# Optimization experiments

Hardware: AMD Instinct MI355X
Metric: run time of the kernel (lower is better)

Reference implementation:

```python
import jax, jax.numpy as jnp
import numpy as np
from jax import lax

B, C, H, W = 16, 512, 16, 300
K, G = 8, 2          # k_clusters, g_clusters (gvlad)
OUT = 5994           # n speakers
DN = ('NCHW', 'OIHW', 'NCHW')


def setup_inputs() -> dict:
    key = jax.random.key(0)
    ks = jax.random.split(key, 10)
    s = lambda fan: 1.0 / np.sqrt(fan)
    return {
        'x5': jax.random.normal(ks[0], (B, C, H, W), jnp.float32),
        'x4': jnp.zeros((1, 1, 1, 1), jnp.float32),
        'x3': jnp.zeros((1, 1, 1, 1), jnp.float32),
        'x2': jnp.zeros((1, 1, 1, 1), jnp.float32),
        'x1': jnp.zeros((1, 1, 1, 1), jnp.float32),
        'conv_w': jax.random.normal(ks[1], (C, C, 7, 1), jnp.float32) * s(C * 7),
        'conv_b': jnp.zeros((C,), jnp.float32),
        'cc_w': jax.random.normal(ks[2], (K + G, C, 7, 1), jnp.float32) * s(C * 7),
        'cc_b': jnp.zeros((K + G,), jnp.float32),
        'centroids': jax.random.normal(ks[3], (K + G, C), jnp.float32),
        'fc_w': jax.random.normal(ks[4], (C, C * K), jnp.float32) * s(C * K),
        'fc_b': jnp.zeros((C,), jnp.float32),
        'logit_w': jax.random.normal(ks[5], (OUT, C), jnp.float32) * s(C),
    }


def _conv(x, w, b=None):
    y = lax.conv_general_dilated(x, w, (1, 1), 'VALID', dimension_numbers=DN)
    if b is not None:
        y = y + b[None, :, None, None]
    return y


def _forward(x5, conv_w, conv_b, cc_w, cc_b, centroids, fc_w, fc_b, logit_w):
    feats = jnp.maximum(_conv(x5, conv_w, conv_b), 0.0)      # (B,C,H',W) relu conv
    scores = _conv(x5, cc_w, cc_b)                           # (B,K+G,H',W)
    assign = jax.nn.softmax(scores, axis=1)                  # soft cluster assignment
    # VLAD: sum_hw a[b,k,h,w]*(f[b,c,h,w] - cent[k,c]), computed without
    # materializing the (B,K+G,C,H',W) residual tensor (same math, fused form)
    agg = jnp.einsum('bkhw,bchw->bkc', assign, feats)        # (B,K+G,C)
    asum = jnp.sum(assign, axis=(2, 3))                      # (B,K+G)
    cluster_res = agg - asum[:, :, None] * centroids[None]   # (B,K+G,C)
    cluster_res = cluster_res[:, :K, :]                      # gvlad: drop ghost clusters
    norm = jnp.linalg.norm(cluster_res, axis=-1, keepdims=True)
    cluster_l2 = cluster_res / jnp.maximum(norm, 1e-12)
    vlad = cluster_l2.reshape(-1, K * C)                     # (B, K*C)
    emb = jnp.maximum(vlad @ fc_w.T + fc_b, 0.0)             # (B,C)
    logit = emb @ logit_w.T                                  # (B,OUT)
    return emb, logit


def reference(x5, x4, x3, x2, x1, conv_w, conv_b, cc_w, cc_b, centroids,
              fc_w, fc_b, logit_w):
    # x4..x1 are unused by Decoder.forward (only x5 flows through)
    return _forward(x5, conv_w, conv_b, cc_w, cc_b, centroids, fc_w, fc_b, logit_w)
```

## Files before the change

### kernel.cpp

```cpp
#include <hip/hip_runtime.h>
#include <hip/hip_bf16.h>

typedef __attribute__((ext_vector_type(8))) short bf16x8;
typedef __attribute__((ext_vector_type(4))) float f32x4;

__device__ __forceinline__ void async16(const void* g, void* l) {
    __builtin_amdgcn_global_load_lds(
        (const __attribute__((address_space(1))) unsigned int*)g,
        (__attribute__((address_space(3))) unsigned int*)l, 16, 0, 0);
}

__global__ __launch_bounds__(256) void pack_all(const float* __restrict__ x5,
                                                const float* __restrict__ conv_w,
                                                const float* __restrict__ cc_w,
                                                __hip_bfloat16* __restrict__ X3,
                                                __hip_bfloat16* __restrict__ A2f) {
    __shared__ __align__(16) float smem[64 * 65];
    const int f = blockIdx.x;
    if (f < 10240) {
        float(*tile)[65] = (float(*)[65])smem;
        const int ct = f / 1280, r = f % 1280;
        const int wt = r >> 8, bh = r & 255;
        const int b = bh >> 4, h = bh & 15;
        const int w0 = wt * 64, c0 = ct * 64;
        const int lw = (threadIdx.x & 15) * 4;
        const int lc = threadIdx.x >> 4;
#pragma unroll
        for (int i = 0; i < 4; ++i) {
            const int c = lc + i * 16;
            const int w = w0 + lw;
            const float* src = &x5[((size_t)(b * 512 + c0 + c) * 16 + h) * 300 + w];
            float4 v = {0.f, 0.f, 0.f, 0.f};
            if (w + 3 < 300) v = *(const float4*)src;
            else {
                if (w < 300)     v.x = src[0];
                if (w + 1 < 300) v.y = src[1];
                if (w + 2 < 300) v.z = src[2];
            }
            *(float4*)&tile[c][lw] = v;
        }
        __syncthreads();
        const int sc = (threadIdx.x & 15) * 4;
        const int sw0 = threadIdx.x >> 4;
#pragma unroll
        for (int i = 0; i < 4; ++i) {
            const int wl = sw0 + i * 16;
            const int w = w0 + wl;
            if (w < 300) {
                __hip_bfloat16 p[4];
                p[0] = __float2bfloat16(tile[sc + 0][wl]);
                p[1] = __float2bfloat16(tile[sc + 1][wl]);
                p[2] = __float2bfloat16(tile[sc + 2][wl]);
                p[3] = __float2bfloat16(tile[sc + 3][wl]);
                *(uint2*)&X3[(((size_t)(b * 16 + h) * 300 + w)) * 512 + c0 + sc] = *(uint2*)p;
            }
        }
    } else {
        float* w = smem;
        const int co = f - 10240;
        if (co < 522) {
            const float4* src = (co < 512) ? (const float4*)(conv_w + (size_t)co * 3584)
                                           : (const float4*)(cc_w + (size_t)(co - 512) * 3584);
            for (int i = threadIdx.x; i < 896; i += 256) *(float4*)&w[i * 4] = src[i];
        } else {
            for (int i = threadIdx.x; i < 3584; i += 256) w[i] = 0.f;
        }
        __syncthreads();
        const int g = co >> 4, fl = co & 15;
        for (int chunk = threadIdx.x; chunk < 448; chunk += 256) {
            const int kk0 = chunk * 8;
            const int kt = kk0 >> 5, sq = (kk0 >> 3) & 3;
            __hip_bfloat16 p[8];
#pragma unroll
            for (int j = 0; j < 8; ++j) {
                const int k = kk0 + j;
                p[j] = __float2bfloat16(w[(k & 511) * 7 + (k >> 9)]);
            }
            char* dst = (char*)A2f + (((size_t)g * 112 + kt) * 64 + sq * 16 + fl) * 16;
            *(uint4*)dst = *(uint4*)p;
        }
    }
}

__global__ __launch_bounds__(256, 4) void conv_gemm(
    const __hip_bfloat16* __restrict__ A2f, const __hip_bfloat16* __restrict__ X3,
    const float* __restrict__ conv_b, const float* __restrict__ cc_b,
    __hip_bfloat16* __restrict__ feats, float* __restrict__ scores) {
    __shared__ __align__(16) char lds[16384];
    const int tid = threadIdx.x;
    const int wv = tid >> 6;
    const int lane = tid & 63;

    const int gid = blockIdx.x;
    const int xcd = gid & 7;
    const int j = gid >> 3;
    const int nb = xcd * 48 + j / 5;
    const int m0 = (j % 5) * 128;
    const int b = nb / 24;
    const int nt = nb % 24;

    const int row0 = wv * 16 + (lane >> 2);
    const int kseg = (lane & 3) ^ ((lane >> 3) & 3);
    int n0 = nt * 128 + row0;      if (n0 > 2999) n0 = 2999;
    int n1 = nt * 128 + row0 + 64; if (n1 > 2999) n1 = 2999;
    const char* gB0 = (const char*)X3 + ((size_t)((b * 16 + n0 / 300) * 300 + n0 % 300)) * 1024 + (size_t)kseg * 16;
    const char* gB1 = (const char*)X3 + ((size_t)((b * 16 + n1 / 300) * 300 + n1 % 300)) * 1024 + (size_t)kseg * 16;
    char* lB = lds + wv * 1024 + lane * 16;

    const int wm = (wv & 1) * 64;
    const int wn = (wv >> 1) * 64;
    const int fl = lane & 15;
    const int sq = lane >> 4;
    int boff[4];
#pragma unroll
    for (int i = 0; i < 4; ++i) {
        const int swz = (sq ^ ((fl >> 1) & 3)) * 16;
        boff[i] = (wn + i * 16 + fl) * 64 + swz;
    }
    const char* Af = (const char*)A2f;
    const int gb = (m0 >> 4) + ((wv & 1) << 2);

    f32x4 acc[4][4] = {};
    bf16x8 aC[4], aN[4];

#define ISSUE_B(kt, ph)                                                                \
    {                                                                                  \
        const size_t badd = (size_t)((kt) >> 4) * 307200 + (size_t)((kt) & 15) * 64;   \
        async16(gB0 + badd, lB + (ph) * 8192);                                         \
        async16(gB1 + badd, lB + (ph) * 8192 + 4096);                                  \
    }
#define PRE_A(kt, arr)                                                                 \
    {                                                                                  \
        _Pragma("unroll")                                                              \
        for (int mi = 0; mi < 4; ++mi)                                                 \
            arr[mi] = *(const bf16x8*)(Af + (((size_t)(gb + mi) * 112 + (kt)) << 10) + (lane << 4)); \
    }
#define COMPUTE(ph, arr)                                                               \
    {                                                                                  \
        _Pragma("unroll")                                                              \
        for (int ni = 0; ni < 4; ++ni) {                                               \
            const bf16x8 bv = *(const bf16x8*)(lds + (ph) * 8192 + boff[ni]);          \
            _Pragma("unroll")                                                          \
            for (int mi = 0; mi < 4; ++mi)                                             \
                acc[mi][ni] = __builtin_amdgcn_mfma_f32_16x16x32_bf16(arr[mi], bv, acc[mi][ni], 0, 0, 0); \
        }                                                                              \
    }

    ISSUE_B(0, 0);
    PRE_A(0, aC);
    for (int kt = 0; kt < 112; kt += 2) {
        __syncthreads();
        ISSUE_B(kt + 1, 1);
        PRE_A(kt + 1, aN);
        COMPUTE(0, aC);
        __syncthreads();
        if (kt < 110) { ISSUE_B(kt + 2, 0); PRE_A(kt + 2, aC); }
        COMPUTE(1, aN);
    }
#undef ISSUE_B
#undef PRE_A
#undef COMPUTE

    const int quad4 = (lane >> 4) * 4;
#pragma unroll
    for (int ni = 0; ni < 4; ++ni) {
        const int n = nt * 128 + wn + ni * 16 + fl;
        if (n >= 3000) continue;
#pragma unroll
        for (int mi = 0; mi < 4; ++mi) {
            const int cob = m0 + wm + mi * 16 + quad4;
            const f32x4 v = acc[mi][ni];
            if (cob < 512) {
                __hip_bfloat16 p[4];
#pragma unroll
                for (int r = 0; r < 4; ++r)
                    p[r] = __float2bfloat16(fmaxf(v[r] + conv_b[cob + r], 0.f));
                *(uint2*)&feats[((size_t)(b * 3000 + n)) * 512 + cob] = *(uint2*)p;
            } else {
#pragma unroll
                for (int r = 0; r < 4; ++r) {
                    const int co = cob + r;
                    if (co < 522)
                        scores[(size_t)(b * 10 + (co - 512)) * 3000 + n] = v[r] + cc_b[co - 512];
                }
            }
        }
    }
}

__global__ __launch_bounds__(256) void softmax_assign(float* __restrict__ scores,
                                                      float* __restrict__ asum_part,
                                                      float* __restrict__ agg) {
    const int b = blockIdx.x;
    const int chunk = blockIdx.y;
    const int zbase = (b * 12 + chunk) * 512 + threadIdx.x;
    if (zbase < 81920) agg[zbase] = 0.f;
    if (zbase + 256 < 81920) agg[zbase + 256] = 0.f;

    const int hw = chunk * 256 + threadIdx.x;
    const bool valid = hw < 3000;
    float part[10];
    if (valid) {
        float s[10], mx = -1e30f;
#pragma unroll
        for (int k = 0; k < 10; ++k) { s[k] = scores[(size_t)(b * 10 + k) * 3000 + hw]; mx = fmaxf(mx, s[k]); }
        float sum = 0.f;
#pragma unroll
        for (int k = 0; k < 10; ++k) { part[k] = __expf(s[k] - mx); sum += part[k]; }
        const float inv = 1.f / sum;
#pragma unroll
        for (int k = 0; k < 10; ++k) {
            part[k] *= inv;
            scores[(size_t)(b * 10 + k) * 3000 + hw] = part[k];
        }
    } else {
#pragma unroll
        for (int k = 0; k < 10; ++k) part[k] = 0.f;
    }
    __shared__ float red[4][10];
    const int lane = threadIdx.x & 63, w = threadIdx.x >> 6;
#pragma unroll
    for (int k = 0; k < 10; ++k) {
        float v = part[k];
        for (int off = 32; off; off >>= 1) v += __shfl_xor(v, off, 64);
        if (lane == 0) red[w][k] = v;
    }
    __syncthreads();
    if (threadIdx.x < 10)
        asum_part[(chunk * 16 + b) * 10 + threadIdx.x] =
            red[0][threadIdx.x] + red[1][threadIdx.x] + red[2][threadIdx.x] + red[3][threadIdx.x];
}

__global__ __launch_bounds__(256) void agg_kernel(const __hip_bfloat16* __restrict__ feats,
                                                  const float* __restrict__ assign,
                                                  float* __restrict__ agg) {
    const int chunk = blockIdx.x, b = blockIdx.y;
    const int c = threadIdx.x * 2;
    float acc0[10], acc1[10];
#pragma unroll
    for (int k = 0; k < 10; ++k) { acc0[k] = 0.f; acc1[k] = 0.f; }
    const int hw0 = chunk * 250;
    for (int i = 0; i < 250; ++i) {
        const int hw = hw0 + i;
        const __hip_bfloat162 f2 = *(const __hip_bfloat162*)&feats[((size_t)(b * 3000 + hw)) * 512 + c];
        const float f0 = __bfloat162float(f2.x), f1 = __bfloat162float(f2.y);
#pragma unroll
        for (int k = 0; k < 10; ++k) {
            const float a = assign[(size_t)(b * 10 + k) * 3000 + hw];
            acc0[k] += a * f0;
            acc1[k] += a * f1;
        }
    }
#pragma unroll
    for (int k = 0; k < 10; ++k) {
        atomicAdd(&agg[(size_t)(b * 10 + k) * 512 + c], acc0[k]);
        atomicAdd(&agg[(size_t)(b * 10 + k) * 512 + c + 1], acc1[k]);
    }
}

__global__ __launch_bounds__(256) void fc_fused(const float* __restrict__ agg,
                                                const float* __restrict__ asum_part,
                                                const float* __restrict__ centroids,
                                                const float* __restrict__ fc_w,
                                                const float* __restrict__ fc_b,
                                                float* __restrict__ out) {
    __shared__ float res[4096];
    __shared__ float sasum[8];
    __shared__ float red[4][8];
    __shared__ float scale[8];
    const int b = blockIdx.y;
    const int t = threadIdx.x;
    if (t < 8) {
        float s = 0.f;
#pragma unroll
        for (int p = 0; p < 12; ++p) s += asum_part[(p * 16 + b) * 10 + t];
        sasum[t] = s;
    }
    __syncthreads();
    float sq[8];
#pragma unroll
    for (int k = 0; k < 8; ++k) sq[k] = 0.f;
#pragma unroll
    for (int jj = 0; jj < 16; ++jj) {
        const int i = t + jj * 256;
        const int k = jj >> 1;
        const int c = i & 511;
        const float r = agg[(size_t)(b * 10 + k) * 512 + c] - sasum[k] * centroids[k * 512 + c];
        res[i] = r;
        sq[k] += r * r;
    }
    const int lane = t & 63, w = t >> 6;
#pragma unroll
    for (int k = 0; k < 8; ++k) {
        float v = sq[k];
        for (int off = 32; off; off >>= 1) v += __shfl_xor(v, off, 64);
        if (lane == 0) red[w][k] = v;
    }
    __syncthreads();
    if (t < 8) {
        const float nrm = sqrtf(red[0][t] + red[1][t] + red[2][t] + red[3][t]);
        scale[t] = 1.f / fmaxf(nrm, 1e-12f);
    }
    __syncthreads();

    const int col = t >> 3;
    const int ks = t & 7;
    const int co = blockIdx.x * 32 + col;
    const float4* w4 = (const float4*)(fc_w + (size_t)co * 4096);
    float acc = 0.f;
    for (int i = ks; i < 1024; i += 8) {
        const float4 wv = w4[i];
        const float4 rv = *(const float4*)&res[i * 4];
        acc += (rv.x * wv.x + rv.y * wv.y + rv.z * wv.z + rv.w * wv.w) * scale[i >> 7];
    }
    acc += __shfl_down(acc, 4, 8);
    acc += __shfl_down(acc, 2, 8);
    acc += __shfl_down(acc, 1, 8);
    if (ks == 0) out[b * 512 + co] = fmaxf(acc + fc_b[co], 0.f);
}

__global__ __launch_bounds__(256) void logit_kernel(const float* __restrict__ emb,
                                                    const float* __restrict__ logit_w,
                                                    float* __restrict__ out) {
    __shared__ float se[512];
    const int gid = blockIdx.x;
    const int xcd = gid & 7;
    const int j = gid >> 3;
    const int otile = xcd * 3 + (j >> 4);
    const int b = j & 15;
    se[threadIdx.x] = emb[b * 512 + threadIdx.x];
    se[threadIdx.x + 256] = emb[b * 512 + threadIdx.x + 256];
    __syncthreads();
    const int o = otile * 256 + threadIdx.x;
    if (o < 5994) {
        const float4* w4 = (const float4*)(logit_w + (size_t)o * 512);
        float acc = 0.f;
        for (int i = 0; i < 128; ++i) {
            const float4 w = w4[i];
            acc += w.x * se[4 * i] + w.y * se[4 * i + 1] + w.z * se[4 * i + 2] + w.w * se[4 * i + 3];
        }
        out[8192 + b * 5994 + o] = acc;
    }
}

extern "C" void kernel_launch(void* const* d_in, const int* in_sizes, int n_in,
                              void* d_out, int out_size, void* d_ws, size_t ws_size,
                              hipStream_t stream) {
    (void)in_sizes; (void)n_in; (void)out_size; (void)ws_size;
    const float* x5       = (const float*)d_in[0];
    const float* conv_w   = (const float*)d_in[5];
    const float* conv_b   = (const float*)d_in[6];
    const float* cc_w     = (const float*)d_in[7];
    const float* cc_b     = (const float*)d_in[8];
    const float* centroids= (const float*)d_in[9];
    const float* fc_w     = (const float*)d_in[10];
    const float* fc_b     = (const float*)d_in[11];
    const float* logit_w  = (const float*)d_in[12];
    float* out = (float*)d_out;

    char* ws = (char*)d_ws;
    __hip_bfloat16* X3    = (__hip_bfloat16*)(ws);
    __hip_bfloat16* A2f   = (__hip_bfloat16*)(ws + 78643200);
    __hip_bfloat16* feats = (__hip_bfloat16*)(ws + 83230720);
    float* scores         = (float*)(ws + 132382720);
    float* asum_part      = (float*)(ws + 134302720);
    float* agg            = (float*)(ws + 134310400);

    pack_all<<<dim3(10880), 256, 0, stream>>>(x5, conv_w, cc_w, X3, A2f);
    conv_gemm<<<dim3(1920), 256, 0, stream>>>(A2f, X3, conv_b, cc_b, feats, scores);
    softmax_assign<<<dim3(16, 12), 256, 0, stream>>>(scores, asum_part, agg);
    agg_kernel<<<dim3(12, 16), 256, 0, stream>>>(feats, scores, agg);
    fc_fused<<<dim3(16, 16), 256, 0, stream>>>(agg, asum_part, centroids, fc_w, fc_b, out);
    logit_kernel<<<dim3(384), 256, 0, stream>>>(out, logit_w, out);
}
```

Measured before the change: 666.4 us.

## Split score GEMM out of conv GEMM to drop padded cluster tile

Before, the fused conv GEMM used a fifth 128-row M tile just to produce 10 cluster-score channels, so most of that tile was wasted MFMA work. Now a separate narrow scores_gemm computes the 10 scores with 16-row tiles over 256 columns, and the conv GEMM covers only the 512 feature channels in two launches of two M tiles each. The agg kernel also splits the hw range into 40 chunks instead of 12 to add parallelism, at the cost of more atomics. The price is extra launches and the X3 activation being read again by the score kernel.

```diff
diff --git a/kernel.cpp b/kernel.cpp
--- a/kernel.cpp
+++ b/kernel.cpp
@@ -84,8 +84,8 @@
 
 __global__ __launch_bounds__(256, 4) void conv_gemm(
     const __hip_bfloat16* __restrict__ A2f, const __hip_bfloat16* __restrict__ X3,
-    const float* __restrict__ conv_b, const float* __restrict__ cc_b,
-    __hip_bfloat16* __restrict__ feats, float* __restrict__ scores) {
+    const float* __restrict__ conv_b,
+    __hip_bfloat16* __restrict__ feats, int m_base) {
     __shared__ __align__(16) char lds[16384];
     const int tid = threadIdx.x;
     const int wv = tid >> 6;
@@ -94,8 +94,8 @@
     const int gid = blockIdx.x;
     const int xcd = gid & 7;
     const int j = gid >> 3;
-    const int nb = xcd * 48 + j / 5;
-    const int m0 = (j % 5) * 128;
+    const int nb = xcd * 48 + (j >> 1);
+    const int m0 = (m_base + (j & 1)) * 128;
     const int b = nb / 24;
     const int nt = nb % 24;
 
@@ -170,20 +170,105 @@
         for (int mi = 0; mi < 4; ++mi) {
             const int cob = m0 + wm + mi * 16 + quad4;
             const f32x4 v = acc[mi][ni];
-            if (cob < 512) {
-                __hip_bfloat16 p[4];
-#pragma unroll
-                for (int r = 0; r < 4; ++r)
-                    p[r] = __float2bfloat16(fmaxf(v[r] + conv_b[cob + r], 0.f));
-                *(uint2*)&feats[((size_t)(b * 3000 + n)) * 512 + cob] = *(uint2*)p;
-            } else {
-#pragma unroll
-                for (int r = 0; r < 4; ++r) {
-                    const int co = cob + r;
-                    if (co < 522)
-                        scores[(size_t)(b * 10 + (co - 512)) * 3000 + n] = v[r] + cc_b[co - 512];
-                }
-            }
+            __hip_bfloat16 p[4];
+#pragma unroll
+            for (int r = 0; r < 4; ++r)
+                p[r] = __float2bfloat16(fmaxf(v[r] + conv_b[cob + r], 0.f));
+            *(uint2*)&feats[((size_t)(b * 3000 + n)) * 512 + cob] = *(uint2*)p;
+        }
+    }
+}
+
+__global__ __launch_bounds__(256) void scores_gemm(
+    const __hip_bfloat16* __restrict__ A2f, const __hip_bfloat16* __restrict__ X3,
+    const float* __restrict__ cc_b, float* __restrict__ scores) {
+    __shared__ __align__(16) char lds[65536];
+    const int tid = threadIdx.x;
+    const int wv = tid >> 6;
+    const int lane = tid & 63;
+    const int gid = blockIdx.x;
+    const int xcd = gid & 7;
+    const int j = gid >> 3;
+    const int b = xcd * 2 + (j >= 12 ? 1 : 0);
+    const int nt2 = j % 12;
+
+    const int row0 = wv * 16 + (lane >> 2);
+    const int kseg = (lane & 3) ^ ((lane >> 3) & 3);
+    const char* gB[4];
+#pragma unroll
+    for (int q = 0; q < 4; ++q) {
+        int n = nt2 * 256 + row0 + q * 64;
+        if (n > 2999) n = 2999;
+        gB[q] = (const char*)X3 + ((size_t)((b * 16 + n / 300) * 300 + n % 300)) * 1024 + (size_t)kseg * 16;
+    }
+    char* lB = lds + wv * 1024 + lane * 16;
+
+    const int wn = wv * 64;
+    const int fl = lane & 15;
+    const int sq = lane >> 4;
+    int boff[4];
+#pragma unroll
+    for (int i = 0; i < 4; ++i) {
+        const int swz = (sq ^ ((fl >> 1) & 3)) * 16;
+        boff[i] = (wn + i * 16 + fl) * 64 + swz;
+    }
+    const char* Af = (const char*)A2f + (((size_t)32 * 112) << 10) + (lane << 4);
+
+    f32x4 acc[4] = {};
+    bf16x8 aC[2], aN[2];
+
+#define S_ISSUE(ktp, ph)                                                               \
+    {                                                                                  \
+        const int kt0 = (ktp) * 2;                                                     \
+        const size_t ba0 = (size_t)(kt0 >> 4) * 307200 + (size_t)(kt0 & 15) * 64;      \
+        const size_t ba1 = (size_t)((kt0 + 1) >> 4) * 307200 + (size_t)((kt0 + 1) & 15) * 64; \
+        _Pragma("unroll")                                                              \
+        for (int q = 0; q < 4; ++q) {                                                  \
+            async16(gB[q] + ba0, lB + (ph) * 32768 + q * 4096);                        \
+            async16(gB[q] + ba1, lB + (ph) * 32768 + 16384 + q * 4096);                \
+        }                                                                              \
+    }
+#define S_PREA(ktp, arr)                                                               \
+    {                                                                                  \
+        arr[0] = *(const bf16x8*)(Af + ((size_t)((ktp) * 2) << 10));                   \
+        arr[1] = *(const bf16x8*)(Af + ((size_t)((ktp) * 2 + 1) << 10));               \
+    }
+#define S_COMP(ph, arr)                                                                \
+    {                                                                                  \
+        _Pragma("unroll")                                                              \
+        for (int kk = 0; kk < 2; ++kk) {                                               \
+            _Pragma("unroll")                                                          \
+            for (int ni = 0; ni < 4; ++ni) {                                           \
+                const bf16x8 bv = *(const bf16x8*)(lds + (ph) * 32768 + kk * 16384 + boff[ni]); \
+                acc[ni] = __builtin_amdgcn_mfma_f32_16x16x32_bf16(arr[kk], bv, acc[ni], 0, 0, 0); \
+            }                                                                          \
+        }                                                                              \
+    }
+
+    S_ISSUE(0, 0);
+    S_PREA(0, aC);
+    for (int ktp = 0; ktp < 56; ktp += 2) {
+        __syncthreads();
+        S_ISSUE(ktp + 1, 1);
+        S_PREA(ktp + 1, aN);
+        S_COMP(0, aC);
+        __syncthreads();
+        if (ktp < 54) { S_ISSUE(ktp + 2, 0); S_PREA(ktp + 2, aC); }
+        S_COMP(1, aN);
+    }
+#undef S_ISSUE
+#undef S_PREA
+#undef S_COMP
+
+#pragma unroll
+    for (int ni = 0; ni < 4; ++ni) {
+        const int n = nt2 * 256 + wn + ni * 16 + fl;
+        if (n >= 3000) continue;
+#pragma unroll
+        for (int r = 0; r < 4; ++r) {
+            const int k = sq * 4 + r;
+            if (k < 10)
+                scores[(size_t)(b * 10 + k) * 3000 + n] = acc[ni][r] + cc_b[k];
         }
     }
 }
@@ -239,8 +324,8 @@
     float acc0[10], acc1[10];
 #pragma unroll
     for (int k = 0; k < 10; ++k) { acc0[k] = 0.f; acc1[k] = 0.f; }
-    const int hw0 = chunk * 250;
-    for (int i = 0; i < 250; ++i) {
+    const int hw0 = chunk * 75;
+    for (int i = 0; i < 75; ++i) {
         const int hw = hw0 + i;
         const __hip_bfloat162 f2 = *(const __hip_bfloat162*)&feats[((size_t)(b * 3000 + hw)) * 512 + c];
         const float f0 = __bfloat162float(f2.x), f1 = __bfloat162float(f2.y);
@@ -367,9 +452,11 @@
     float* agg            = (float*)(ws + 134310400);
 
     pack_all<<<dim3(10880), 256, 0, stream>>>(x5, conv_w, cc_w, X3, A2f);
-    conv_gemm<<<dim3(1920), 256, 0, stream>>>(A2f, X3, conv_b, cc_b, feats, scores);
+    scores_gemm<<<dim3(192), 256, 0, stream>>>(A2f, X3, cc_b, scores);
     softmax_assign<<<dim3(16, 12), 256, 0, stream>>>(scores, asum_part, agg);
-    agg_kernel<<<dim3(12, 16), 256, 0, stream>>>(feats, scores, agg);
+    conv_gemm<<<dim3(768), 256, 0, stream>>>(A2f, X3, conv_b, feats, 0);
+    conv_gemm<<<dim3(768), 256, 0, stream>>>(A2f, X3, conv_b, feats, 2);
+    agg_kernel<<<dim3(40, 16), 256, 0, stream>>>(feats, scores, agg);
     fc_fused<<<dim3(16, 16), 256, 0, stream>>>(agg, asum_part, centroids, fc_w, fc_b, out);
     logit_kernel<<<dim3(384), 256, 0, stream>>>(out, logit_w, out);
 }
```

Result: faster. 653.1 us (-2.0%).
